# Kernel tuning notes

Hardware: AMD Instinct MI355X
Metric: run time of the kernel (lower is better)

## Reference

```python
import jax, jax.numpy as jnp
import numpy as np

# config (matches init_kwargs)
B, H, N, D = 2, 8, 2048, 64
ALPHA = 1.0        # < 2 -> power-law kernel branch
D_INT = 4.0        # d_intrinsic
BW = 1.0           # bandwidth
A = 0.5            # dual-sided degree-normalization exponent
R = 1.0            # sphere_radius
MASK_VAL = 10000.0
EPS = 1e-7


def setup_inputs() -> dict:
    key = jax.random.key(0)
    k1, k2, k3, k4 = jax.random.split(key, 4)
    Q = jax.random.normal(k1, (B, H, N, D), dtype=jnp.float32)
    K = jax.random.normal(k2, (B, H, N, D), dtype=jnp.float32)
    V = jax.random.normal(k3, (B, H, N, D), dtype=jnp.float32)
    mask = jax.random.randint(k4, (B, N), 0, 2).astype(jnp.int32)
    return {"Q": Q, "K": K, "V": V, "mask": mask}


def reference(Q, K, V, mask) -> jnp.ndarray:
    # geodesic distance on the sphere: acos(clamp(QK^T)) * radius  [B,H,N,N]
    qk = jnp.einsum('bhnd,bhmd->bhnm', Q, K)
    g_dist = jnp.arccos(jnp.clip(qk, -1.0 + EPS, 1.0 - EPS)) * R
    # key-side padding mask: [B,N] -> [B,1,1,N]
    g_dist = jnp.where(mask[:, None, None, :] == 0, MASK_VAL, g_dist)
    # power-law kernel (alpha < 2 branch)
    attn_score = (1.0 + g_dist / jnp.sqrt(BW)) ** (-D_INT - ALPHA)
    # dual-sided degree normalization (a != 0 branch)
    n_r = jnp.sum(attn_score, axis=-1)   # row degrees [B,H,N]
    n_c = jnp.sum(attn_score, axis=-2)   # col degrees [B,H,N]
    k_tilde = (n_r ** (-A))[..., :, None] * attn_score * (n_c ** (-A))[..., None, :]
    # F.normalize(p=1, dim=3)
    attn = k_tilde / jnp.maximum(jnp.sum(jnp.abs(k_tilde), axis=-1, keepdims=True), 1e-12)
    # dropout p=0.0 -> identity
    return jnp.einsum('bhnm,bhmd->bhnd', attn, V)
```

## Files before the change

### kernel.cpp

```cpp
#include <hip/hip_runtime.h>
#include <hip/hip_bf16.h>
#include <math.h>

#define B_ 2
#define H_ 8
#define N_ 2048
#define D_ 64
#define BH_ 16
#define NT_ (N_/64)
#define LS 72
#define LSW (LS/2)

typedef __attribute__((ext_vector_type(8))) short short8;
typedef __attribute__((ext_vector_type(4))) float float4v;

__device__ __forceinline__ unsigned packbf2(float a, float b){
  __hip_bfloat162 h = __float22bfloat162_rn(make_float2(a, b));
  return *(unsigned*)&h;
}
__device__ __forceinline__ void split2(float a, float b, unsigned& hi, unsigned& lo){
  hi = packbf2(a, b);
  float ha = __uint_as_float(hi << 16);
  float hb = __uint_as_float(hi & 0xFFFF0000u);
  lo = packbf2(a - ha, b - hb);
}
__device__ __forceinline__ void load_split8(const float* p, short8& hi8, short8& lo8){
  float4v v0 = *(const float4v*)p;
  float4v v1 = *(const float4v*)(p + 4);
  unsigned h0,h1,h2,h3,l0,l1,l2,l3;
  split2(v0.x, v0.y, h0, l0);
  split2(v0.z, v0.w, h1, l1);
  split2(v1.x, v1.y, h2, l2);
  split2(v1.z, v1.w, h3, l3);
  unsigned ph[4] = {h0,h1,h2,h3};
  unsigned pl[4] = {l0,l1,l2,l3};
  hi8 = *(short8*)ph;
  lo8 = *(short8*)pl;
}

__device__ __forceinline__ float score_fn(float qk, float masked){
  float ax = fminf(fabsf(qk), 1.0f - 1e-7f);
  float t  = __builtin_amdgcn_sqrtf(1.0f - ax);
  float p  = __builtin_fmaf(__builtin_fmaf(__builtin_fmaf(-0.0187293f, ax, 0.0742610f),
                                           ax, -0.2121144f), ax, 1.5707288f);
  float t2 = t * p;
  float g  = (qk >= 0.0f) ? t2 : (3.14159265358979f - t2);
  g = (masked != 0.0f) ? 10000.0f : g;
  float w1 = 1.0f + g;
  float w2 = w1*w1;
  float w4 = w2*w2;
  float w5 = w4*w1;
  return __builtin_amdgcn_rcpf(w5);
}

template<bool STORE>
__global__ __launch_bounds__(256) void k1_score(
    const float* __restrict__ Q, const float* __restrict__ K,
    const int* __restrict__ mask, float* __restrict__ ncw,
    unsigned short* __restrict__ S)
{
  __shared__ float msk[64];
  __shared__ float red[64*4];

  const int kt = blockIdx.x, bh = blockIdx.y, rz = blockIdx.z;
  const int nz = gridDim.z;
  const int tid = threadIdx.x;
  const int wv = tid>>6, lane = tid&63, quad = lane>>4, l15 = lane&15;

  const float* Qg = Q + (size_t)bh*N_*D_;
  const float* Kg = K + (size_t)bh*N_*D_;

  short8 khi[4][2], klo[4][2];
  #pragma unroll
  for (int s=0;s<4;++s){
    const float* kp = Kg + (size_t)(kt*64 + s*16 + l15)*D_ + quad*8;
    load_split8(kp,      khi[s][0], klo[s][0]);
    load_split8(kp + 32, khi[s][1], klo[s][1]);
  }
  if (tid < 64)
    msk[tid] = (mask[(bh>>3)*N_ + kt*64 + tid] == 0) ? 1.f : 0.f;
  __syncthreads();

  float cs[4][4];
  #pragma unroll
  for (int s=0;s<4;++s)
    #pragma unroll
    for (int i=0;i<4;++i) cs[s][i] = 0.f;

  const int iters = NT_/nz;
  for (int rti=0; rti<iters; ++rti){
    const int rt = rz*iters + rti;
    const float* qp = Qg + (size_t)(rt*64 + wv*16 + l15)*D_ + quad*8;
    short8 bhi[2], blo[2];
    load_split8(qp,      bhi[0], blo[0]);
    load_split8(qp + 32, bhi[1], blo[1]);

    const size_t nrow = (size_t)(bh*NT_ + kt)*N_ + (size_t)rt*64 + wv*16 + l15;
    #pragma unroll
    for (int s=0;s<4;++s){
      float4v c = {0.f,0.f,0.f,0.f};
      #pragma unroll
      for (int cc=0; cc<2; ++cc){
        c = __builtin_amdgcn_mfma_f32_16x16x32_bf16(khi[s][cc], bhi[cc], c, 0,0,0);
        c = __builtin_amdgcn_mfma_f32_16x16x32_bf16(khi[s][cc], blo[cc], c, 0,0,0);
        c = __builtin_amdgcn_mfma_f32_16x16x32_bf16(klo[s][cc], bhi[cc], c, 0,0,0);
      }
      int kl = s*16 + quad*4;
      float sc0 = score_fn(c[0], msk[kl+0]);
      float sc1 = score_fn(c[1], msk[kl+1]);
      float sc2 = score_fn(c[2], msk[kl+2]);
      float sc3 = score_fn(c[3], msk[kl+3]);
      cs[s][0]+=sc0; cs[s][1]+=sc1; cs[s][2]+=sc2; cs[s][3]+=sc3;
      if (STORE){
        uint2 pk;
        pk.x = packbf2(sc0, sc1);
        pk.y = packbf2(sc2, sc3);
        *(uint2*)&S[nrow*64 + kl] = pk;
      }
    }
  }

  #pragma unroll
  for (int s=0;s<4;++s)
    #pragma unroll
    for (int i=0;i<4;++i){
      float v2 = cs[s][i];
      v2 += __shfl_xor(v2, 1);
      v2 += __shfl_xor(v2, 2);
      v2 += __shfl_xor(v2, 4);
      v2 += __shfl_xor(v2, 8);
      cs[s][i] = v2;
    }
  if (l15 == 0){
    #pragma unroll
    for (int s=0;s<4;++s)
      #pragma unroll
      for (int i=0;i<4;++i)
        red[(s*16 + quad*4 + i)*4 + wv] = cs[s][i];
  }
  __syncthreads();
  if (tid < 64){
    float t = red[tid*4+0] + red[tid*4+1] + red[tid*4+2] + red[tid*4+3];
    if (STORE) atomicAdd(&ncw[bh*N_ + kt*64 + tid], t);
    else       ncw[bh*N_ + kt*64 + tid] = 1.0f / sqrtf(t);
  }
}

__global__ __launch_bounds__(256) void k2_pack(
    const float* __restrict__ V, const float* __restrict__ nc,
    unsigned short* __restrict__ Vw)
{
  __shared__ float T[64*65];
  __shared__ float wrow[64];
  const int mt = blockIdx.x, bh = blockIdx.y;
  const int tid = threadIdx.x;
  const float* Vg = V + (size_t)bh*N_*D_;
  const float* ncg = nc + (size_t)bh*N_;
  unsigned short* Fb = Vw + ((size_t)(bh*NT_ + mt)*10)*512;

  {
    int m = tid >> 2;
    int d0 = (tid & 3) * 16;
    int gm = mt*64 + m;
    float wm = 1.0f / sqrtf(fmaxf(ncg[gm], 1e-30f));
    if (d0 == 0) wrow[m] = wm;
    #pragma unroll
    for (int j=0;j<4;++j){
      float4v v = *(const float4v*)(Vg + (size_t)gm*D_ + d0 + j*4);
      T[(d0+j*4+0)*65 + m] = v.x*wm;
      T[(d0+j*4+1)*65 + m] = v.y*wm;
      T[(d0+j*4+2)*65 + m] = v.z*wm;
      T[(d0+j*4+3)*65 + m] = v.w*wm;
    }
  }
  __syncthreads();

  for (int idx = tid; idx < 640; idx += 256){
    int f = idx >> 6, lane = idx & 63;
    int quad = lane >> 4, l15 = lane & 15;
    int s2 = f >> 1, cc = f & 1;
    int m0 = cc*32 + quad*8;
    unsigned pk[4];
    if (s2 < 4){
      int d = s2*16 + l15;
      #pragma unroll
      for (int j=0;j<4;++j)
        pk[j] = packbf2(T[d*65 + m0 + 2*j], T[d*65 + m0 + 2*j + 1]);
    } else if (l15 == 0){
      #pragma unroll
      for (int j=0;j<4;++j)
        pk[j] = packbf2(wrow[m0 + 2*j], wrow[m0 + 2*j + 1]);
    } else {
      pk[0]=pk[1]=pk[2]=pk[3]=0u;
    }
    *(short8*)(Fb + ((size_t)f*64 + lane)*8) = *(short8*)pk;
  }
}

__global__ __launch_bounds__(1024) void k3_stream(
    const unsigned short* __restrict__ S, const unsigned short* __restrict__ Vw,
    float* __restrict__ out)
{
  __shared__ float Red[4*3*16*68];

  const int rt = blockIdx.x, bh = blockIdx.y;
  const int tid = threadIdx.x;
  const int wvid = tid >> 6;
  const int sr = wvid & 3;
  const int kc = wvid >> 2;
  const int lane = tid & 63, quad = lane>>4, l15 = lane&15;

  float4v acc[4];
  #pragma unroll
  for (int i=0;i<4;++i) acc[i] = (float4v){0.f,0.f,0.f,0.f};
  float4v c5 = {0.f,0.f,0.f,0.f};

  const size_t srow = (size_t)rt*64 + sr*16 + l15;

  short8 npf0[2], npf1[2];
  #pragma unroll
  for (int d2=0; d2<2; ++d2){
    const size_t sb = ((size_t)(bh*NT_ + kc*8 + d2)*N_ + srow)*64;
    npf0[d2] = *(const short8*)&S[sb +  0 + quad*8];
    npf1[d2] = *(const short8*)&S[sb + 32 + quad*8];
  }

  for (int ki=0; ki<8; ++ki){
    const int kt = kc*8 + ki;
    const int cur = ki & 1;
    short8 pf0 = npf0[cur], pf1 = npf1[cur];
    if (ki < 6){
      const size_t sb = ((size_t)(bh*NT_ + kt + 2)*N_ + srow)*64;
      npf0[cur] = *(const short8*)&S[sb +  0 + quad*8];
      npf1[cur] = *(const short8*)&S[sb + 32 + quad*8];
    }
    const unsigned short* F = Vw + ((size_t)(bh*NT_ + kt)*10)*512 + (size_t)lane*8;
    short8 va[10];
    #pragma unroll
    for (int f=0; f<10; ++f)
      va[f] = *(const short8*)(F + (size_t)f*512);

    #pragma unroll
    for (int s2=0;s2<4;++s2){
      acc[s2] = __builtin_amdgcn_mfma_f32_16x16x32_bf16(va[s2*2+0], pf0, acc[s2], 0,0,0);
      acc[s2] = __builtin_amdgcn_mfma_f32_16x16x32_bf16(va[s2*2+1], pf1, acc[s2], 0,0,0);
    }
    c5 = __builtin_amdgcn_mfma_f32_16x16x32_bf16(va[8], pf0, c5, 0,0,0);
    c5 = __builtin_amdgcn_mfma_f32_16x16x32_bf16(va[9], pf1, c5, 0,0,0);
  }

  if (kc > 0){
    float* Rr = Red + ((size_t)((sr*3 + (kc-1))*16) + l15)*68;
    #pragma unroll
    for (int s2=0;s2<4;++s2)
      #pragma unroll
      for (int i=0;i<4;++i)
        Rr[s2*16 + quad*4 + i] = acc[s2][i];
    if (quad == 0) Rr[64] = c5[0];
  }
  __syncthreads();
  if (kc == 0){
    #pragma unroll
    for (int p=0; p<3; ++p){
      const float* Rr = Red + ((size_t)((sr*3 + p)*16) + l15)*68;
      #pragma unroll
      for (int s2=0;s2<4;++s2)
        #pragma unroll
        for (int i=0;i<4;++i)
          acc[s2][i] += Rr[s2*16 + quad*4 + i];
    }
    float rs = __shfl(c5[0], l15);
    #pragma unroll
    for (int p=0; p<3; ++p)
      rs += Red[((size_t)((sr*3 + p)*16) + l15)*68 + 64];
    float inv = 1.0f / fmaxf(rs, 1e-12f);

    float* Og = out + (size_t)bh*N_*D_ + (size_t)(rt*64 + sr*16 + l15)*D_;
    #pragma unroll
    for (int s2=0;s2<4;++s2)
      #pragma unroll
      for (int i=0;i<4;++i)
        Og[s2*16 + quad*4 + i] = acc[s2][i] * inv;
  }
}

__global__ __launch_bounds__(256) void spop_pass2(
    const float* __restrict__ Q, const float* __restrict__ K,
    const float* __restrict__ V, const int* __restrict__ mask,
    const float* __restrict__ w, float* __restrict__ out)
{
  __shared__ unsigned short Khi[64*LS], Klo[64*LS];
  __shared__ unsigned short Vt[64*LS];
  __shared__ unsigned short Ps[64*LS];
  __shared__ float msk[64], wms[64];

  const int rt = blockIdx.x, bh = blockIdx.y, b = bh>>3;
  const int tid = threadIdx.x;
  const int wv = tid>>6, lane = tid&63, quad = lane>>4, l15 = lane&15;

  const float* Qg = Q + (size_t)bh*N_*D_;
  const float* Kg = K + (size_t)bh*N_*D_;
  const float* Vg = V + (size_t)bh*N_*D_;

  short8 qhi[2], qlo[2];
  {
    const float* qp = Qg + (size_t)(rt*64 + wv*16 + l15)*D_ + quad*8;
    load_split8(qp,      qhi[0], qlo[0]);
    load_split8(qp + 32, qhi[1], qlo[1]);
  }

  float4v acc[4];
  #pragma unroll
  for (int i=0;i<4;++i) acc[i] = (float4v){0.f,0.f,0.f,0.f};
  float rs = 0.f;

  for (int kt=0; kt<NT_; ++kt){
    __syncthreads();
    #pragma unroll
    for (int it=0; it<4; ++it){
      int idx = tid + it*256;
      int r = idx>>4, d4 = (idx&15)<<2;
      const float4v v = *(const float4v*)(Kg + (size_t)(kt*64 + r)*D_ + d4);
      unsigned h0,l0,h1,l1;
      split2(v.x, v.y, h0, l0);
      split2(v.z, v.w, h1, l1);
      unsigned* KhiW = (unsigned*)Khi; unsigned* KloW = (unsigned*)Klo;
      int base = r*LSW + (d4>>1);
      KhiW[base] = h0; KhiW[base+1] = h1;
      KloW[base] = l0; KloW[base+1] = l1;
    }
    #pragma unroll
    for (int it=0; it<2; ++it){
      int u = tid + it*256;
      int kp = u & 31;
      int d4 = (u>>5)<<2;
      const float* vp = Vg + (size_t)(kt*64 + kp*2)*D_ + d4;
      float4v a0 = *(const float4v*)vp;
      float4v a1 = *(const float4v*)(vp + D_);
      unsigned* VtW = (unsigned*)Vt;
      VtW[(d4+0)*LSW + kp] = packbf2(a0.x, a1.x);
      VtW[(d4+1)*LSW + kp] = packbf2(a0.y, a1.y);
      VtW[(d4+2)*LSW + kp] = packbf2(a0.z, a1.z);
      VtW[(d4+3)*LSW + kp] = packbf2(a0.w, a1.w);
    }
    if (tid < 64){
      int gk = kt*64 + tid;
      msk[tid] = (mask[b*N_ + gk] == 0) ? 1.f : 0.f;
      wms[tid] = w[bh*N_ + gk];
    }
    __syncthreads();

    #pragma unroll
    for (int s=0;s<4;++s){
      float4v c = {0.f,0.f,0.f,0.f};
      #pragma unroll
      for (int cc=0; cc<2; ++cc){
        const short8 ahi = *(const short8*)&Khi[(s*16+l15)*LS + cc*32 + quad*8];
        const short8 alo = *(const short8*)&Klo[(s*16+l15)*LS + cc*32 + quad*8];
        c = __builtin_amdgcn_mfma_f32_16x16x32_bf16(ahi, qhi[cc], c, 0,0,0);
        c = __builtin_amdgcn_mfma_f32_16x16x32_bf16(ahi, qlo[cc], c, 0,0,0);
        c = __builtin_amdgcn_mfma_f32_16x16x32_bf16(alo, qhi[cc], c, 0,0,0);
      }
      int kl = s*16 + quad*4;
      float sc0 = score_fn(c[0], msk[kl+0]) * wms[kl+0];
      float sc1 = score_fn(c[1], msk[kl+1]) * wms[kl+1];
      float sc2 = score_fn(c[2], msk[kl+2]) * wms[kl+2];
      float sc3 = score_fn(c[3], msk[kl+3]) * wms[kl+3];
      rs += (sc0 + sc1) + (sc2 + sc3);
      unsigned* PsW = (unsigned*)Ps;
      int pb = (wv*16 + l15)*LSW + (kl>>1);
      PsW[pb]   = packbf2(sc0, sc1);
      PsW[pb+1] = packbf2(sc2, sc3);
    }

    short8 pf[2];
    pf[0] = *(const short8*)&Ps[(wv*16+l15)*LS +  0 + quad*8];
    pf[1] = *(const short8*)&Ps[(wv*16+l15)*LS + 32 + quad*8];
    #pragma unroll
    for (int s2=0;s2<4;++s2){
      #pragma unroll
      for (int cc=0; cc<2; ++cc){
        const short8 av = *(const short8*)&Vt[(s2*16+l15)*LS + cc*32 + quad*8];
        acc[s2] = __builtin_amdgcn_mfma_f32_16x16x32_bf16(av, pf[cc], acc[s2], 0,0,0);
      }
    }
  }

  rs += __shfl_xor(rs, 16);
  rs += __shfl_xor(rs, 32);
  float inv = 1.0f / fmaxf(rs, 1e-12f);

  float* Og = out + (size_t)bh*N_*D_ + (size_t)(rt*64 + wv*16 + l15)*D_;
  #pragma unroll
  for (int s2=0;s2<4;++s2)
    #pragma unroll
    for (int i=0;i<4;++i)
      Og[s2*16 + quad*4 + i] = acc[s2][i] * inv;
}

extern "C" void kernel_launch(void* const* d_in, const int* in_sizes, int n_in,
                              void* d_out, int out_size, void* d_ws, size_t ws_size,
                              hipStream_t stream) {
  (void)in_sizes; (void)n_in; (void)out_size;
  const float* Q   = (const float*)d_in[0];
  const float* K   = (const float*)d_in[1];
  const float* V   = (const float*)d_in[2];
  const int*  mask = (const int*)d_in[3];
  float* out = (float*)d_out;

  const size_t nc_bytes = (size_t)BH_*N_*sizeof(float);
  const size_t vw_off   = 131072;
  const size_t vw_bytes = (size_t)BH_*NT_*10*512*2;
  const size_t s_off    = vw_off + vw_bytes;
  const size_t S_bytes  = (size_t)2*BH_*N_*N_;
  const size_t need     = s_off + S_bytes;

  if (ws_size >= need){
    float* nc = (float*)d_ws;
    unsigned short* Vw = (unsigned short*)((char*)d_ws + vw_off);
    unsigned short* S  = (unsigned short*)((char*)d_ws + s_off);
    hipMemsetAsync(nc, 0, nc_bytes, stream);
    k1_score<true><<<dim3(NT_, BH_, 4), 256, 0, stream>>>(Q, K, mask, nc, S);
    k2_pack<<<dim3(NT_, BH_), 256, 0, stream>>>(V, nc, Vw);
    k3_stream<<<dim3(NT_, BH_), 1024, 0, stream>>>(S, Vw, out);
  } else {
    float* w = (float*)d_ws;
    k1_score<false><<<dim3(NT_, BH_, 1), 256, 0, stream>>>(Q, K, mask, w, nullptr);
    spop_pass2<<<dim3(NT_, BH_), 256, 0, stream>>>(Q, K, V, mask, w, out);
  }
}
```

Measured before the change: 193.4 us.

## Stage packed V tiles in LDS and share across 128-row blocks in k3

```diff
diff --git a/kernel.cpp b/kernel.cpp
--- a/kernel.cpp
+++ b/kernel.cpp
@@ -197,48 +197,63 @@
   }
 }
 
-__global__ __launch_bounds__(1024) void k3_stream(
+__global__ __launch_bounds__(1024) void k3_lds(
     const unsigned short* __restrict__ S, const unsigned short* __restrict__ Vw,
     float* __restrict__ out)
 {
-  __shared__ float Red[4*3*16*68];
-
-  const int rt = blockIdx.x, bh = blockIdx.y;
+  __shared__ unsigned short Vs[2*2*10*512];
+
+  const int rtp = blockIdx.x, bh = blockIdx.y;
   const int tid = threadIdx.x;
   const int wvid = tid >> 6;
-  const int sr = wvid & 3;
-  const int kc = wvid >> 2;
-  const int lane = tid & 63, quad = lane>>4, l15 = lane&15;
+  const int g    = wvid >> 3;
+  const int slot = wvid & 7;
+  const int lane = tid & 63, quad = lane >> 4, l15 = lane & 15;
+
+  const int row = rtp*128 + slot*16 + l15;
 
   float4v acc[4];
   #pragma unroll
   for (int i=0;i<4;++i) acc[i] = (float4v){0.f,0.f,0.f,0.f};
   float4v c5 = {0.f,0.f,0.f,0.f};
 
-  const size_t srow = (size_t)rt*64 + sr*16 + l15;
-
-  short8 npf0[2], npf1[2];
-  #pragma unroll
-  for (int d2=0; d2<2; ++d2){
-    const size_t sb = ((size_t)(bh*NT_ + kc*8 + d2)*N_ + srow)*64;
-    npf0[d2] = *(const short8*)&S[sb +  0 + quad*8];
-    npf1[d2] = *(const short8*)&S[sb + 32 + quad*8];
-  }
-
-  for (int ki=0; ki<8; ++ki){
-    const int kt = kc*8 + ki;
-    const int cur = ki & 1;
-    short8 pf0 = npf0[cur], pf1 = npf1[cur];
-    if (ki < 6){
-      const size_t sb = ((size_t)(bh*NT_ + kt + 2)*N_ + srow)*64;
-      npf0[cur] = *(const short8*)&S[sb +  0 + quad*8];
-      npf1[cur] = *(const short8*)&S[sb + 32 + quad*8];
-    }
-    const unsigned short* F = Vw + ((size_t)(bh*NT_ + kt)*10)*512 + (size_t)lane*8;
+  for (int c = tid; c < 1280; c += 1024){
+    const int gg = (c >= 640) ? 1 : 0;
+    const int rem = c - gg*640;
+    const int f = rem >> 6, ln = rem & 63;
+    const int kt = gg*16;
+    *(short8*)&Vs[(((0*2 + gg)*10 + f) << 9) + ln*8] =
+      *(const short8*)&Vw[(((size_t)(bh*NT_ + kt)*10 + f) << 9) + ln*8];
+  }
+  short8 npf0, npf1;
+  {
+    const size_t sb = ((size_t)(bh*NT_ + g*16)*N_ + row)*64;
+    npf0 = *(const short8*)&S[sb + quad*8];
+    npf1 = *(const short8*)&S[sb + 32 + quad*8];
+  }
+  __syncthreads();
+
+  for (int it = 0; it < 16; ++it){
+    const int cur = it & 1, nxt = cur ^ 1;
+    short8 pf0 = npf0, pf1 = npf1;
+    if (it < 15){
+      const size_t sb = ((size_t)(bh*NT_ + g*16 + it + 1)*N_ + row)*64;
+      npf0 = *(const short8*)&S[sb + quad*8];
+      npf1 = *(const short8*)&S[sb + 32 + quad*8];
+      for (int c = tid; c < 1280; c += 1024){
+        const int gg = (c >= 640) ? 1 : 0;
+        const int rem = c - gg*640;
+        const int f = rem >> 6, ln = rem & 63;
+        const int kt2 = gg*16 + it + 1;
+        *(short8*)&Vs[(((nxt*2 + gg)*10 + f) << 9) + ln*8] =
+          *(const short8*)&Vw[(((size_t)(bh*NT_ + kt2)*10 + f) << 9) + ln*8];
+      }
+    }
+    const unsigned short* Fl = &Vs[((cur*2 + g)*10) << 9] + (size_t)lane*8;
     short8 va[10];
     #pragma unroll
     for (int f=0; f<10; ++f)
-      va[f] = *(const short8*)(F + (size_t)f*512);
+      va[f] = *(const short8*)(Fl + ((size_t)f << 9));
 
     #pragma unroll
     for (int s2=0;s2<4;++s2){
@@ -247,10 +262,13 @@
     }
     c5 = __builtin_amdgcn_mfma_f32_16x16x32_bf16(va[8], pf0, c5, 0,0,0);
     c5 = __builtin_amdgcn_mfma_f32_16x16x32_bf16(va[9], pf1, c5, 0,0,0);
-  }
-
-  if (kc > 0){
-    float* Rr = Red + ((size_t)((sr*3 + (kc-1))*16) + l15)*68;
+
+    __syncthreads();
+  }
+
+  float* Red = (float*)Vs;
+  if (g == 1){
+    float* Rr = Red + (size_t)(slot*16 + l15)*68;
     #pragma unroll
     for (int s2=0;s2<4;++s2)
       #pragma unroll
@@ -259,23 +277,17 @@
     if (quad == 0) Rr[64] = c5[0];
   }
   __syncthreads();
-  if (kc == 0){
-    #pragma unroll
-    for (int p=0; p<3; ++p){
-      const float* Rr = Red + ((size_t)((sr*3 + p)*16) + l15)*68;
-      #pragma unroll
-      for (int s2=0;s2<4;++s2)
-        #pragma unroll
-        for (int i=0;i<4;++i)
-          acc[s2][i] += Rr[s2*16 + quad*4 + i];
-    }
-    float rs = __shfl(c5[0], l15);
-    #pragma unroll
-    for (int p=0; p<3; ++p)
-      rs += Red[((size_t)((sr*3 + p)*16) + l15)*68 + 64];
+  if (g == 0){
+    const float* Rr = Red + (size_t)(slot*16 + l15)*68;
+    #pragma unroll
+    for (int s2=0;s2<4;++s2)
+      #pragma unroll
+      for (int i=0;i<4;++i)
+        acc[s2][i] += Rr[s2*16 + quad*4 + i];
+    float rs = __shfl(c5[0], l15) + Rr[64];
     float inv = 1.0f / fmaxf(rs, 1e-12f);
 
-    float* Og = out + (size_t)bh*N_*D_ + (size_t)(rt*64 + sr*16 + l15)*D_;
+    float* Og = out + (size_t)bh*N_*D_ + (size_t)row*D_;
     #pragma unroll
     for (int s2=0;s2<4;++s2)
       #pragma unroll
@@ -422,7 +434,7 @@
     hipMemsetAsync(nc, 0, nc_bytes, stream);
     k1_score<true><<<dim3(NT_, BH_, 4), 256, 0, stream>>>(Q, K, mask, nc, S);
     k2_pack<<<dim3(NT_, BH_), 256, 0, stream>>>(V, nc, Vw);
-    k3_stream<<<dim3(NT_, BH_), 1024, 0, stream>>>(S, Vw, out);
+    k3_lds<<<dim3(N_/128, BH_), 1024, 0, stream>>>(S, Vw, out);
   } else {
     float* w = (float*)d_ws;
     k1_score<false><<<dim3(NT_, BH_, 1), 256, 0, stream>>>(Q, K, mask, w, nullptr);
```

Result: faster. 188.9 us (-2.4%).
